# Kernel optimization log

Hardware: AMD Instinct MI355X
Metric: run time of the kernel (lower is better)

Reference implementation:

```python
import jax, jax.numpy as jnp
import numpy as np

EPS = 1e-7

def safe_divide(num, den):
    safe_den = jnp.where(jnp.abs(den) > EPS, den, jnp.sign(den) * EPS)
    return num / safe_den

def mlp(x, W1, b1, W2, b2):
    return jnp.tanh(x @ W1 + b1) @ W2 + b2

B, L, C, H, T = 16384, 256, 512, 1024, 16

def setup_inputs() -> dict:
    key = jax.random.key(0)
    ks = jax.random.split(key, 12)
    s = 0.05
    z = jax.random.normal(ks[0], (B, 2 * L + 1), dtype=jnp.float32)
    ctx = jax.random.normal(ks[1], (B, T, C), dtype=jnp.float32)
    ts = jnp.arange(T, dtype=jnp.float32) * 0.1  # sorted time knots
    t = jnp.float32(0.75)                        # solver query time
    inverse_mass = jnp.ones((1, L), dtype=jnp.float32)
    # fixed diffusion = sqrt(2*gamma/beta), gamma=1, beta=1/3 -> sqrt(6)
    diffusion = jnp.full((1, L), np.sqrt(6.0), dtype=jnp.float32)
    # control_network: Linear(2L+C -> H), tanh, Linear(H -> L)
    Wc1 = jax.random.normal(ks[2], (2 * L + C, H), dtype=jnp.float32) * s
    bc1 = jnp.zeros((H,), dtype=jnp.float32)
    Wc2 = jax.random.normal(ks[3], (H, L), dtype=jnp.float32) * s
    bc2 = jnp.zeros((L,), dtype=jnp.float32)
    # h_net (prior drift): Linear(2L -> H), tanh, Linear(H -> L)
    Wh1 = jax.random.normal(ks[4], (2 * L, H), dtype=jnp.float32) * s
    bh1 = jnp.zeros((H,), dtype=jnp.float32)
    Wh2 = jax.random.normal(ks[5], (H, L), dtype=jnp.float32) * s
    bh2 = jnp.zeros((L,), dtype=jnp.float32)
    return {"z": z, "ts": ts, "t": t, "ctx": ctx,
            "inverse_mass": inverse_mass, "diffusion": diffusion,
            "Wc1": Wc1, "bc1": bc1, "Wc2": Wc2, "bc2": bc2,
            "Wh1": Wh1, "bh1": bh1, "Wh2": Wh2, "bh2": bh2}

def reference(z, ts, t, ctx, inverse_mass, diffusion,
              Wc1, bc1, Wc2, bc2, Wh1, bh1, Wh2, bh2):
    # f_and_g_absolute: one drift/diffusion evaluation of the second-order latent SDE
    pm = z[..., :-1]                      # [B, 2L] position+momentum
    momentum = pm[..., pm.shape[-1] // 2:]  # [B, L]
    # context lookup via searchsorted(right) clamped to last knot
    i = jnp.minimum(jnp.searchsorted(ts, t, side='right'), ts.shape[0] - 1)
    position_drift = inverse_mass * momentum                      # [B, L]
    prior_momentum_drift = mlp(pm, Wh1, bh1, Wh2, bh2)            # [B, L]
    posterior_momentum_drift = mlp(
        jnp.concatenate([pm, ctx[:, i]], axis=-1), Wc1, bc1, Wc2, bc2)  # [B, L]
    difference = prior_momentum_drift - posterior_momentum_drift
    momentum_diffusion = jnp.broadcast_to(diffusion, (z.shape[0], diffusion.shape[-1]))
    dkl_drift = jnp.sum(jnp.square(safe_divide(difference, momentum_diffusion)),
                        axis=-1, keepdims=True)                   # [B, 1]
    drift = jnp.concatenate([position_drift, posterior_momentum_drift, dkl_drift], axis=-1)
    diffusion_out = jnp.concatenate(
        [jnp.zeros_like(momentum_diffusion), momentum_diffusion,
         jnp.zeros_like(dkl_drift)], axis=-1)
    return drift, diffusion_out
```

## Files before the change

kernel.cpp:

```cpp
#include <hip/hip_runtime.h>

typedef __attribute__((ext_vector_type(8))) short short8;
typedef __attribute__((ext_vector_type(4))) float f32x4;

#define AS1 __attribute__((address_space(1)))
#define AS3 __attribute__((address_space(3)))

#define NB 16384
#define LDIM 256
#define CDIM 512
#define HDIM 1024

__device__ __forceinline__ unsigned short f2bf(float x) {
    unsigned u = __float_as_uint(x);
    u += 0x7fffu + ((u >> 16) & 1u);
    return (unsigned short)(u >> 16);
}

__device__ __forceinline__ void gld_lds16(const unsigned short* g, unsigned short* l) {
    __builtin_amdgcn_global_load_lds((const AS1 void*)g, (AS3 void*)l, 16, 0, 0);
}

__device__ __forceinline__ float tanh_fast(float x) {
    x = fminf(fmaxf(x, -15.f), 15.f);
    float e = __expf(2.f * x);
    return (e - 1.f) * __builtin_amdgcn_rcpf(e + 1.f);
}

__global__ __launch_bounds__(256)
void build_w(const float* __restrict__ Wc1, const float* __restrict__ bc1,
             const float* __restrict__ Wc2, const float* __restrict__ bc2,
             const float* __restrict__ Wh1, const float* __restrict__ bh1,
             const float* __restrict__ Wh2, const float* __restrict__ bh2,
             unsigned short* __restrict__ W1T, unsigned short* __restrict__ W2T,
             float* __restrict__ bias1, float* __restrict__ bias2)
{
    __shared__ float s[64][65];
    const int bid = blockIdx.x;
    const int tid = threadIdx.x;

    if (bid >= 640) {
        int id = (bid - 640) * 256 + tid;
        if (id < 2048)      bias1[id] = (id < 1024) ? bc1[id] : bh1[id - 1024];
        else if (id < 2560) { int n = id - 2048; bias2[n] = (n < 256) ? bc2[n] : bh2[n - 256]; }
        return;
    }

    const int tk = bid & 15;
    const int k0 = tk * 64;
    const float* src; int srcStride, n0s, kmax, dn0;
    unsigned short* dst;
    if (bid < 512) {
        const int tn = bid >> 4;
        dst = W1T; dn0 = tn * 64; srcStride = 1024;
        if (tn < 16) { src = Wc1; n0s = tn * 64;        kmax = 1024; }
        else         { src = Wh1; n0s = (tn - 16) * 64; kmax = 512;  }
    } else {
        const int tn = (bid - 512) >> 4;
        dst = W2T; dn0 = tn * 64; srcStride = 256;
        if (tn < 4) { src = Wc2; n0s = tn * 64;       kmax = 1024; }
        else        { src = Wh2; n0s = (tn - 4) * 64; kmax = 1024; }
    }

    #pragma unroll
    for (int rd = 0; rd < 4; ++rd) {
        int e = rd * 1024 + tid * 4;
        int r = e >> 6;
        int c = e & 63;
        f32x4 v = {0.f, 0.f, 0.f, 0.f};
        int k = k0 + r;
        if (k < kmax) v = *(const f32x4*)(src + (size_t)k * srcStride + n0s + c);
        s[r][c + 0] = v[0]; s[r][c + 1] = v[1]; s[r][c + 2] = v[2]; s[r][c + 3] = v[3];
    }
    __syncthreads();

    #pragma unroll
    for (int wr = 0; wr < 2; ++wr) {
        int e = wr * 2048 + tid * 8;
        int on = e >> 6;
        int ok = e & 63;
        short8 o;
        #pragma unroll
        for (int j = 0; j < 8; ++j) o[j] = (short)f2bf(s[ok + j][on]);
        *(short8*)(dst + (size_t)(dn0 + on) * 1024 + k0 + ok) = o;
    }
}

__global__ void build_A1(const float* __restrict__ z, const float* __restrict__ ts,
                         const float* __restrict__ t, const float* __restrict__ ctx,
                         const float* __restrict__ im, const float* __restrict__ dfu,
                         unsigned short* __restrict__ A1, float* __restrict__ out)
{
    __shared__ int sh_i;
    if (threadIdx.x == 0) {
        float tv = t[0];
        int c = 0;
        #pragma unroll
        for (int q = 0; q < 16; ++q) c += (ts[q] <= tv) ? 1 : 0;
        sh_i = (c < 15) ? c : 15;
    }
    __syncthreads();
    const int i = sh_i;
    size_t id = (size_t)blockIdx.x * 256 + threadIdx.x;
    int b  = (int)(id >> 7);
    int c0 = ((int)id & 127) << 3;
    short8 v;
    if (c0 < 512) {
        const float* zp = z + (size_t)b * 513 + c0;
        float zv[8];
        #pragma unroll
        for (int q = 0; q < 8; ++q) zv[q] = zp[q];
        #pragma unroll
        for (int q = 0; q < 8; ++q) v[q] = (short)f2bf(zv[q]);
        float* drift = out + (size_t)b * 513;
        float* dif   = out + (size_t)NB * 513 + (size_t)b * 513;
        if (c0 < 256) {
            #pragma unroll
            for (int q = 0; q < 8; ++q) dif[c0 + q] = 0.f;
        } else {
            int mc = c0 - 256;
            #pragma unroll
            for (int q = 0; q < 8; ++q) {
                drift[mc + q] = im[mc + q] * zv[q];
                dif[c0 + q]   = dfu[mc + q];
            }
        }
    } else {
        const f32x4* cp = (const f32x4*)(ctx + ((size_t)b * 16 + i) * 512 + (c0 - 512));
        f32x4 x0 = cp[0], x1 = cp[1];
        #pragma unroll
        for (int q = 0; q < 4; ++q) { v[q] = (short)f2bf(x0[q]); v[4 + q] = (short)f2bf(x1[q]); }
    }
    *(short8*)(A1 + id * 8) = v;
    if (id < NB) {
        out[id * 513 + 512] = 0.f;
        out[(size_t)NB * 513 + id * 513 + 512] = 0.f;
    }
}

__global__ __launch_bounds__(256)
void gemm1(const unsigned short* __restrict__ A, const unsigned short* __restrict__ BT,
           const float* __restrict__ bias, unsigned short* __restrict__ Hout)
{
    __shared__ unsigned short sA[128 * 32];
    __shared__ unsigned short sB[128 * 32];

    const int tid  = threadIdx.x;
    const int lane = tid & 63;
    const int wave = tid >> 6;

    int lin = blockIdx.y * 16 + blockIdx.x;
    lin = (lin & 7) * 256 + (lin >> 3);
    const int ntile = lin & 15;
    const int mtile = lin >> 4;
    const int kdim  = (ntile < 8) ? 1024 : 512;

    const int m0 = mtile * 128;
    const int n0 = ntile * 128;

    const int row0 = tid >> 2,         cb0 = tid & 3;
    const int row1 = (256 + tid) >> 2, cb1 = (256 + tid) & 3;

    const unsigned short* aG0 = A + (size_t)(m0 + row0) * 1024 + cb0 * 8;
    const unsigned short* aG1 = A + (size_t)(m0 + row1) * 1024 + cb1 * 8;
    const unsigned short* bG0 = BT + (size_t)(n0 + row0) * 1024 + cb0 * 8;
    const unsigned short* bG1 = BT + (size_t)(n0 + row1) * 1024 + cb1 * 8;

    unsigned short* sA0 = sA + (size_t)(wave * 64) * 8;
    unsigned short* sA1 = sA + (size_t)(256 + wave * 64) * 8;
    unsigned short* sB0 = sB + (size_t)(wave * 64) * 8;
    unsigned short* sB1 = sB + (size_t)(256 + wave * 64) * 8;

    const int wm = (wave & 1) * 64;
    const int wn = (wave >> 1) * 64;
    const int lr = lane & 15;
    const int kq = (lane >> 4) * 8;

    f32x4 acc[4][4] = {};

    for (int k0 = 0; k0 < kdim; k0 += 32) {
        gld_lds16(aG0 + k0, sA0);
        gld_lds16(aG1 + k0, sA1);
        gld_lds16(bG0 + k0, sB0);
        gld_lds16(bG1 + k0, sB1);
        __syncthreads();

        short8 af[4], bfr[4];
        #pragma unroll
        for (int i = 0; i < 4; ++i)
            af[i] = *(const short8*)&sA[(wm + i * 16 + lr) * 32 + kq];
        #pragma unroll
        for (int i = 0; i < 4; ++i)
            bfr[i] = *(const short8*)&sB[(wn + i * 16 + lr) * 32 + kq];

        #pragma unroll
        for (int i = 0; i < 4; ++i)
            #pragma unroll
            for (int j = 0; j < 4; ++j)
                acc[i][j] = __builtin_amdgcn_mfma_f32_16x16x32_bf16(af[i], bfr[j], acc[i][j], 0, 0, 0);
        __syncthreads();
    }

    const int rquad = (lane >> 4) * 4;
    #pragma unroll
    for (int i = 0; i < 4; ++i) {
        const int gr = m0 + wm + i * 16 + rquad;
        #pragma unroll
        for (int j = 0; j < 4; ++j) {
            const int gc = n0 + wn + j * 16 + lr;
            const float bs = bias[gc];
            #pragma unroll
            for (int r = 0; r < 4; ++r) {
                float x = acc[i][j][r] + bs;
                Hout[(size_t)(gr + r) * 2048 + gc] = f2bf(tanh_fast(x));
            }
        }
    }
}

__global__ __launch_bounds__(512)
void gemm2_fused(const unsigned short* __restrict__ Hm, const unsigned short* __restrict__ W2T,
                 const float* __restrict__ bias2, const float* __restrict__ dfu,
                 float* __restrict__ out)
{
    __shared__ unsigned short sAp[64 * 32];
    __shared__ unsigned short sAq[64 * 32];
    __shared__ unsigned short sBp[128 * 32];
    __shared__ unsigned short sBq[128 * 32];

    const int tid  = threadIdx.x;
    const int lane = tid & 63;
    const int w    = tid >> 6;

    int lin = blockIdx.y * 2 + blockIdx.x;
    lin = (lin & 7) * 64 + (lin >> 3);
    const int n0 = (lin & 1) * 128;
    const int m0 = (lin >> 1) * 64;

    const int srow = lane >> 2;
    const int cb   = lane & 3;
    const int aseg = w & 3;
    const unsigned short* aG = Hm + (size_t)(m0 + aseg * 16 + srow) * 2048
                                  + ((w >> 2) ? 1024 : 0) + cb * 8;
    unsigned short* aL = ((w >> 2) ? sAq : sAp) + aseg * 512;
    const unsigned short* bpG = W2T + (size_t)(n0 + w * 16 + srow) * 1024 + cb * 8;
    const unsigned short* bqG = bpG + 256 * 1024;
    unsigned short* bpL = sBp + w * 512;
    unsigned short* bqL = sBq + w * 512;

    const int wn = w * 16;
    const int lr = lane & 15;
    const int kq = (lane >> 4) * 8;

    f32x4 accp[4] = {};
    f32x4 accq[4] = {};

    for (int k0 = 0; k0 < 1024; k0 += 32) {
        gld_lds16(aG  + k0, aL);
        gld_lds16(bpG + k0, bpL);
        gld_lds16(bqG + k0, bqL);
        __syncthreads();

        short8 afp[4], afq[4], bp, bq;
        #pragma unroll
        for (int i = 0; i < 4; ++i) {
            afp[i] = *(const short8*)&sAp[(i * 16 + lr) * 32 + kq];
            afq[i] = *(const short8*)&sAq[(i * 16 + lr) * 32 + kq];
        }
        bp = *(const short8*)&sBp[(wn + lr) * 32 + kq];
        bq = *(const short8*)&sBq[(wn + lr) * 32 + kq];

        #pragma unroll
        for (int i = 0; i < 4; ++i) {
            accp[i] = __builtin_amdgcn_mfma_f32_16x16x32_bf16(afp[i], bp, accp[i], 0, 0, 0);
            accq[i] = __builtin_amdgcn_mfma_f32_16x16x32_bf16(afq[i], bq, accq[i], 0, 0, 0);
        }
        __syncthreads();
    }

    const int gc = n0 + wn + lr;
    const float bcv = bias2[gc];
    const float bhv = bias2[256 + gc];
    float d   = dfu[gc];
    float sgn = (d > 0.f) ? 1.f : ((d < 0.f) ? -1.f : 0.f);
    float sd  = (fabsf(d) > 1e-7f) ? d : sgn * 1e-7f;
    const int rquad = (lane >> 4) * 4;

    #pragma unroll
    for (int i = 0; i < 4; ++i) {
        #pragma unroll
        for (int r = 0; r < 4; ++r) {
            const int gr = m0 + i * 16 + rquad + r;
            float post = accp[i][r] + bcv;
            float pri  = accq[i][r] + bhv;
            out[(size_t)gr * 513 + 256 + gc] = post;
            float qq = (pri - post) / sd;
            float s2 = qq * qq;
            #pragma unroll
            for (int m = 1; m < 16; m <<= 1) s2 += __shfl_xor(s2, m, 64);
            if (lr == 0) atomicAdd(&out[(size_t)gr * 513 + 512], s2);
        }
    }
}

extern "C" void kernel_launch(void* const* d_in, const int* in_sizes, int n_in,
                              void* d_out, int out_size, void* d_ws, size_t ws_size,
                              hipStream_t stream) {
    const float* z    = (const float*)d_in[0];
    const float* ts   = (const float*)d_in[1];
    const float* t    = (const float*)d_in[2];
    const float* ctx  = (const float*)d_in[3];
    const float* im   = (const float*)d_in[4];
    const float* dfu  = (const float*)d_in[5];
    const float* Wc1  = (const float*)d_in[6];
    const float* bc1  = (const float*)d_in[7];
    const float* Wc2  = (const float*)d_in[8];
    const float* bc2  = (const float*)d_in[9];
    const float* Wh1  = (const float*)d_in[10];
    const float* bh1  = (const float*)d_in[11];
    const float* Wh2  = (const float*)d_in[12];
    const float* bh2  = (const float*)d_in[13];

    char* ws = (char*)d_ws;
    unsigned short* A1  = (unsigned short*)(ws);
    unsigned short* H   = (unsigned short*)(ws + 33554432ull);
    unsigned short* W1T = (unsigned short*)(ws + 100663296ull);
    unsigned short* W2T = (unsigned short*)(ws + 104857600ull);
    float*          b1  = (float*)(ws + 105906176ull);
    float*          b2  = (float*)(ws + 105914368ull);

    float* out = (float*)d_out;

    build_w<<<650, 256, 0, stream>>>(Wc1, bc1, Wc2, bc2, Wh1, bh1, Wh2, bh2, W1T, W2T, b1, b2);
    build_A1<<<8192, 256, 0, stream>>>(z, ts, t, ctx, im, dfu, A1, out);

    dim3 g1(16, 128);
    gemm1<<<g1, 256, 0, stream>>>(A1, W1T, b1, H);

    dim3 g2(2, 256);
    gemm2_fused<<<g2, 512, 0, stream>>>(H, W2T, b2, dfu, out);
}
```

Baseline: 773.1 us.

## Merge prep kernels, double K-tile depth in GEMMs, load gemm2 B from global

Merges the weight-transpose and activation-pack kernels into one launch, which removes a kernel launch and lets the two pieces of work overlap. Both GEMMs now stage K tiles of 64 instead of 32, halving the number of barrier pairs per K loop. gemm2 reads its B fragments straight from global memory into registers instead of staging them in LDS. The larger LDS tiles and the direct global B loads may hurt occupancy or add load latency that is not hidden.

```diff
diff --git a/kernel.cpp b/kernel.cpp
--- a/kernel.cpp
+++ b/kernel.cpp
@@ -28,71 +28,67 @@
 }
 
 __global__ __launch_bounds__(256)
-void build_w(const float* __restrict__ Wc1, const float* __restrict__ bc1,
-             const float* __restrict__ Wc2, const float* __restrict__ bc2,
-             const float* __restrict__ Wh1, const float* __restrict__ bh1,
-             const float* __restrict__ Wh2, const float* __restrict__ bh2,
-             unsigned short* __restrict__ W1T, unsigned short* __restrict__ W2T,
-             float* __restrict__ bias1, float* __restrict__ bias2)
+void prep(const float* __restrict__ z, const float* __restrict__ ts,
+          const float* __restrict__ t, const float* __restrict__ ctx,
+          const float* __restrict__ im, const float* __restrict__ dfu,
+          const float* __restrict__ Wc1, const float* __restrict__ bc1,
+          const float* __restrict__ Wc2, const float* __restrict__ bc2,
+          const float* __restrict__ Wh1, const float* __restrict__ bh1,
+          const float* __restrict__ Wh2, const float* __restrict__ bh2,
+          unsigned short* __restrict__ A1, float* __restrict__ out,
+          unsigned short* __restrict__ W1T, unsigned short* __restrict__ W2T,
+          float* __restrict__ bias1, float* __restrict__ bias2)
 {
     __shared__ float s[64][65];
-    const int bid = blockIdx.x;
+    __shared__ int sh_i;
     const int tid = threadIdx.x;
 
-    if (bid >= 640) {
-        int id = (bid - 640) * 256 + tid;
-        if (id < 2048)      bias1[id] = (id < 1024) ? bc1[id] : bh1[id - 1024];
-        else if (id < 2560) { int n = id - 2048; bias2[n] = (n < 256) ? bc2[n] : bh2[n - 256]; }
+    if (blockIdx.x >= 8192) {
+        const int bid = (int)blockIdx.x - 8192;
+        if (bid >= 640) {
+            int id = (bid - 640) * 256 + tid;
+            if (id < 2048)      bias1[id] = (id < 1024) ? bc1[id] : bh1[id - 1024];
+            else if (id < 2560) { int n = id - 2048; bias2[n] = (n < 256) ? bc2[n] : bh2[n - 256]; }
+            return;
+        }
+        const int tk = bid & 15;
+        const int k0 = tk * 64;
+        const float* src; int srcStride, n0s, kmax, dn0;
+        unsigned short* dst;
+        if (bid < 512) {
+            const int tn = bid >> 4;
+            dst = W1T; dn0 = tn * 64; srcStride = 1024;
+            if (tn < 16) { src = Wc1; n0s = tn * 64;        kmax = 1024; }
+            else         { src = Wh1; n0s = (tn - 16) * 64; kmax = 512;  }
+        } else {
+            const int tn = (bid - 512) >> 4;
+            dst = W2T; dn0 = tn * 64; srcStride = 256;
+            if (tn < 4) { src = Wc2; n0s = tn * 64;       kmax = 1024; }
+            else        { src = Wh2; n0s = (tn - 4) * 64; kmax = 1024; }
+        }
+        #pragma unroll
+        for (int rd = 0; rd < 4; ++rd) {
+            int e = rd * 1024 + tid * 4;
+            int r = e >> 6, c = e & 63;
+            f32x4 v = {0.f, 0.f, 0.f, 0.f};
+            int k = k0 + r;
+            if (k < kmax) v = *(const f32x4*)(src + (size_t)k * srcStride + n0s + c);
+            s[r][c + 0] = v[0]; s[r][c + 1] = v[1]; s[r][c + 2] = v[2]; s[r][c + 3] = v[3];
+        }
+        __syncthreads();
+        #pragma unroll
+        for (int wr = 0; wr < 2; ++wr) {
+            int e = wr * 2048 + tid * 8;
+            int on = e >> 6, ok = e & 63;
+            short8 o;
+            #pragma unroll
+            for (int j = 0; j < 8; ++j) o[j] = (short)f2bf(s[ok + j][on]);
+            *(short8*)(dst + (size_t)(dn0 + on) * 1024 + k0 + ok) = o;
+        }
         return;
     }
 
-    const int tk = bid & 15;
-    const int k0 = tk * 64;
-    const float* src; int srcStride, n0s, kmax, dn0;
-    unsigned short* dst;
-    if (bid < 512) {
-        const int tn = bid >> 4;
-        dst = W1T; dn0 = tn * 64; srcStride = 1024;
-        if (tn < 16) { src = Wc1; n0s = tn * 64;        kmax = 1024; }
-        else         { src = Wh1; n0s = (tn - 16) * 64; kmax = 512;  }
-    } else {
-        const int tn = (bid - 512) >> 4;
-        dst = W2T; dn0 = tn * 64; srcStride = 256;
-        if (tn < 4) { src = Wc2; n0s = tn * 64;       kmax = 1024; }
-        else        { src = Wh2; n0s = (tn - 4) * 64; kmax = 1024; }
-    }
-
-    #pragma unroll
-    for (int rd = 0; rd < 4; ++rd) {
-        int e = rd * 1024 + tid * 4;
-        int r = e >> 6;
-        int c = e & 63;
-        f32x4 v = {0.f, 0.f, 0.f, 0.f};
-        int k = k0 + r;
-        if (k < kmax) v = *(const f32x4*)(src + (size_t)k * srcStride + n0s + c);
-        s[r][c + 0] = v[0]; s[r][c + 1] = v[1]; s[r][c + 2] = v[2]; s[r][c + 3] = v[3];
-    }
-    __syncthreads();
-
-    #pragma unroll
-    for (int wr = 0; wr < 2; ++wr) {
-        int e = wr * 2048 + tid * 8;
-        int on = e >> 6;
-        int ok = e & 63;
-        short8 o;
-        #pragma unroll
-        for (int j = 0; j < 8; ++j) o[j] = (short)f2bf(s[ok + j][on]);
-        *(short8*)(dst + (size_t)(dn0 + on) * 1024 + k0 + ok) = o;
-    }
-}
-
-__global__ void build_A1(const float* __restrict__ z, const float* __restrict__ ts,
-                         const float* __restrict__ t, const float* __restrict__ ctx,
-                         const float* __restrict__ im, const float* __restrict__ dfu,
-                         unsigned short* __restrict__ A1, float* __restrict__ out)
-{
-    __shared__ int sh_i;
-    if (threadIdx.x == 0) {
+    if (tid == 0) {
         float tv = t[0];
         int c = 0;
         #pragma unroll
@@ -101,7 +97,7 @@
     }
     __syncthreads();
     const int i = sh_i;
-    size_t id = (size_t)blockIdx.x * 256 + threadIdx.x;
+    size_t id = (size_t)blockIdx.x * 256 + tid;
     int b  = (int)(id >> 7);
     int c0 = ((int)id & 127) << 3;
     short8 v;
@@ -142,8 +138,8 @@
 void gemm1(const unsigned short* __restrict__ A, const unsigned short* __restrict__ BT,
            const float* __restrict__ bias, unsigned short* __restrict__ Hout)
 {
-    __shared__ unsigned short sA[128 * 32];
-    __shared__ unsigned short sB[128 * 32];
+    __shared__ unsigned short sA[128 * 64];
+    __shared__ unsigned short sB[128 * 64];
 
     const int tid  = threadIdx.x;
     const int lane = tid & 63;
@@ -158,18 +154,12 @@
     const int m0 = mtile * 128;
     const int n0 = ntile * 128;
 
-    const int row0 = tid >> 2,         cb0 = tid & 3;
-    const int row1 = (256 + tid) >> 2, cb1 = (256 + tid) & 3;
-
-    const unsigned short* aG0 = A + (size_t)(m0 + row0) * 1024 + cb0 * 8;
-    const unsigned short* aG1 = A + (size_t)(m0 + row1) * 1024 + cb1 * 8;
-    const unsigned short* bG0 = BT + (size_t)(n0 + row0) * 1024 + cb0 * 8;
-    const unsigned short* bG1 = BT + (size_t)(n0 + row1) * 1024 + cb1 * 8;
-
-    unsigned short* sA0 = sA + (size_t)(wave * 64) * 8;
-    unsigned short* sA1 = sA + (size_t)(256 + wave * 64) * 8;
-    unsigned short* sB0 = sB + (size_t)(wave * 64) * 8;
-    unsigned short* sB1 = sB + (size_t)(256 + wave * 64) * 8;
+    const int srow = tid >> 3;
+    const int sc   = (tid & 7) * 8;
+    const unsigned short* aG = A  + (size_t)(m0 + srow) * 1024 + sc;
+    const unsigned short* bG = BT + (size_t)(n0 + srow) * 1024 + sc;
+    unsigned short* const sAb = sA + wave * 512;
+    unsigned short* const sBb = sB + wave * 512;
 
     const int wm = (wave & 1) * 64;
     const int wn = (wave >> 1) * 64;
@@ -178,26 +168,30 @@
 
     f32x4 acc[4][4] = {};
 
-    for (int k0 = 0; k0 < kdim; k0 += 32) {
-        gld_lds16(aG0 + k0, sA0);
-        gld_lds16(aG1 + k0, sA1);
-        gld_lds16(bG0 + k0, sB0);
-        gld_lds16(bG1 + k0, sB1);
-        __syncthreads();
-
-        short8 af[4], bfr[4];
-        #pragma unroll
-        for (int i = 0; i < 4; ++i)
-            af[i] = *(const short8*)&sA[(wm + i * 16 + lr) * 32 + kq];
-        #pragma unroll
-        for (int i = 0; i < 4; ++i)
-            bfr[i] = *(const short8*)&sB[(wn + i * 16 + lr) * 32 + kq];
-
-        #pragma unroll
-        for (int i = 0; i < 4; ++i)
-            #pragma unroll
-            for (int j = 0; j < 4; ++j)
-                acc[i][j] = __builtin_amdgcn_mfma_f32_16x16x32_bf16(af[i], bfr[j], acc[i][j], 0, 0, 0);
+    for (int k0 = 0; k0 < kdim; k0 += 64) {
+        #pragma unroll
+        for (int r = 0; r < 4; ++r) {
+            gld_lds16(aG + (size_t)r * 32 * 1024 + k0, sAb + r * 2048);
+            gld_lds16(bG + (size_t)r * 32 * 1024 + k0, sBb + r * 2048);
+        }
+        __syncthreads();
+
+        #pragma unroll
+        for (int kk = 0; kk < 64; kk += 32) {
+            short8 af[4], bfr[4];
+            #pragma unroll
+            for (int i = 0; i < 4; ++i)
+                af[i] = *(const short8*)&sA[(wm + i * 16 + lr) * 64 + kk + kq];
+            #pragma unroll
+            for (int i = 0; i < 4; ++i)
+                bfr[i] = *(const short8*)&sB[(wn + i * 16 + lr) * 64 + kk + kq];
+
+            #pragma unroll
+            for (int i = 0; i < 4; ++i)
+                #pragma unroll
+                for (int j = 0; j < 4; ++j)
+                    acc[i][j] = __builtin_amdgcn_mfma_f32_16x16x32_bf16(af[i], bfr[j], acc[i][j], 0, 0, 0);
+        }
         __syncthreads();
     }
 
@@ -223,10 +217,8 @@
                  const float* __restrict__ bias2, const float* __restrict__ dfu,
                  float* __restrict__ out)
 {
-    __shared__ unsigned short sAp[64 * 32];
-    __shared__ unsigned short sAq[64 * 32];
-    __shared__ unsigned short sBp[128 * 32];
-    __shared__ unsigned short sBq[128 * 32];
+    __shared__ unsigned short sAp[64 * 64];
+    __shared__ unsigned short sAq[64 * 64];
 
     const int tid  = threadIdx.x;
     const int lane = tid & 63;
@@ -237,43 +229,53 @@
     const int n0 = (lin & 1) * 128;
     const int m0 = (lin >> 1) * 64;
 
-    const int srow = lane >> 2;
-    const int cb   = lane & 3;
-    const int aseg = w & 3;
-    const unsigned short* aG = Hm + (size_t)(m0 + aseg * 16 + srow) * 2048
-                                  + ((w >> 2) ? 1024 : 0) + cb * 8;
-    unsigned short* aL = ((w >> 2) ? sAq : sAp) + aseg * 512;
-    const unsigned short* bpG = W2T + (size_t)(n0 + w * 16 + srow) * 1024 + cb * 8;
-    const unsigned short* bqG = bpG + 256 * 1024;
-    unsigned short* bpL = sBp + w * 512;
-    unsigned short* bqL = sBq + w * 512;
+    const int srow = tid >> 3;
+    const int sc   = (tid & 7) * 8;
+    const unsigned short* aGp = Hm + (size_t)(m0 + srow) * 2048 + sc;
+    const unsigned short* aGq = aGp + 1024;
+    unsigned short* const aLp = sAp + w * 512;
+    unsigned short* const aLq = sAq + w * 512;
 
     const int wn = w * 16;
     const int lr = lane & 15;
     const int kq = (lane >> 4) * 8;
 
+    const unsigned short* bPr = W2T + (size_t)(n0 + wn + lr) * 1024 + kq;
+    const unsigned short* bQr = bPr + 256 * 1024;
+
     f32x4 accp[4] = {};
     f32x4 accq[4] = {};
 
-    for (int k0 = 0; k0 < 1024; k0 += 32) {
-        gld_lds16(aG  + k0, aL);
-        gld_lds16(bpG + k0, bpL);
-        gld_lds16(bqG + k0, bqL);
-        __syncthreads();
-
-        short8 afp[4], afq[4], bp, bq;
+    for (int k0 = 0; k0 < 1024; k0 += 64) {
+        short8 bp0 = *(const short8*)(bPr + k0);
+        short8 bp1 = *(const short8*)(bPr + k0 + 32);
+        short8 bq0 = *(const short8*)(bQr + k0);
+        short8 bq1 = *(const short8*)(bQr + k0 + 32);
+
+        gld_lds16(aGp + k0, aLp);
+        gld_lds16(aGq + k0, aLq);
+        __syncthreads();
+
+        short8 afp[4], afq[4];
         #pragma unroll
         for (int i = 0; i < 4; ++i) {
-            afp[i] = *(const short8*)&sAp[(i * 16 + lr) * 32 + kq];
-            afq[i] = *(const short8*)&sAq[(i * 16 + lr) * 32 + kq];
-        }
-        bp = *(const short8*)&sBp[(wn + lr) * 32 + kq];
-        bq = *(const short8*)&sBq[(wn + lr) * 32 + kq];
-
+            afp[i] = *(const short8*)&sAp[(i * 16 + lr) * 64 + kq];
+            afq[i] = *(const short8*)&sAq[(i * 16 + lr) * 64 + kq];
+        }
         #pragma unroll
         for (int i = 0; i < 4; ++i) {
-            accp[i] = __builtin_amdgcn_mfma_f32_16x16x32_bf16(afp[i], bp, accp[i], 0, 0, 0);
-            accq[i] = __builtin_amdgcn_mfma_f32_16x16x32_bf16(afq[i], bq, accq[i], 0, 0, 0);
+            accp[i] = __builtin_amdgcn_mfma_f32_16x16x32_bf16(afp[i], bp0, accp[i], 0, 0, 0);
+            accq[i] = __builtin_amdgcn_mfma_f32_16x16x32_bf16(afq[i], bq0, accq[i], 0, 0, 0);
+        }
+        #pragma unroll
+        for (int i = 0; i < 4; ++i) {
+            afp[i] = *(const short8*)&sAp[(i * 16 + lr) * 64 + 32 + kq];
+            afq[i] = *(const short8*)&sAq[(i * 16 + lr) * 64 + 32 + kq];
+        }
+        #pragma unroll
+        for (int i = 0; i < 4; ++i) {
+            accp[i] = __builtin_amdgcn_mfma_f32_16x16x32_bf16(afp[i], bp1, accp[i], 0, 0, 0);
+            accq[i] = __builtin_amdgcn_mfma_f32_16x16x32_bf16(afq[i], bq1, accq[i], 0, 0, 0);
         }
         __syncthreads();
     }
@@ -331,8 +333,9 @@
 
     float* out = (float*)d_out;
 
-    build_w<<<650, 256, 0, stream>>>(Wc1, bc1, Wc2, bc2, Wh1, bh1, Wh2, bh2, W1T, W2T, b1, b2);
-    build_A1<<<8192, 256, 0, stream>>>(z, ts, t, ctx, im, dfu, A1, out);
+    prep<<<8842, 256, 0, stream>>>(z, ts, t, ctx, im, dfu,
+                                   Wc1, bc1, Wc2, bc2, Wh1, bh1, Wh2, bh2,
+                                   A1, out, W1T, W2T, b1, b2);
 
     dim3 g1(16, 128);
     gemm1<<<g1, 256, 0, stream>>>(A1, W1T, b1, H);
```

Result: no change. 781.7 us (+1.1%).
